# Kernel optimization log

Hardware: AMD Instinct MI355X
Metric: run time of the kernel (lower is better)

## Reference

```python
import jax, jax.numpy as jnp
import numpy as np

NUM_STEPS = 100
STEP = 2.0 / (NUM_STEPS - 1)          # bin width over [-1, 1]
EPS = 1.0 / NUM_STEPS
TSIZE = NUM_STEPS                      # bin centers t_k = -1 + k*STEP, k=0..99
B, D = 4096, 128
NUM_CLASSES = 100


def setup_inputs() -> dict:
    key = jax.random.key(0)
    k1, k2 = jax.random.split(key)
    embeddings = jax.random.normal(k1, (B, D), dtype=jnp.float32)
    classes = jax.random.randint(k2, (B,), 0, NUM_CLASSES)
    return {"embeddings": embeddings, "classes": classes}


def _histogram_loss(embeddings, classes):
    n = embeddings.shape[0]
    iu, ju = np.triu_indices(n, 1)            # static upper-triangular pair indices
    # cosine similarity of all pairs (outer_cosine_similarity)
    en = embeddings / jnp.linalg.norm(embeddings, axis=1, keepdims=True)
    dists = en @ en.T                          # [B, B]
    s = jnp.clip(dists[iu, ju], -1.0 + 1e-6, 1.0 - 1e-6)   # [P]
    pos = (classes[iu] == classes[ju])         # [P] bool

    # soft triangular-kernel 2-bin scatter (equivalent to indsa/indsb masking):
    # bin j gets (t_j + STEP - s)/STEP, bin j+1 gets (s - t_j)/STEP
    j = jnp.floor((s + 1.0 - 1e-6) / STEP).astype(jnp.int32)   # lower bin index
    t_j = j.astype(s.dtype) * STEP - 1.0
    w_hi = (s - t_j) / STEP                    # weight for bin j+1
    w_lo = (t_j + STEP - s) / STEP             # weight for bin j

    def histogram(mask):
        m = mask.astype(s.dtype)
        size = m.sum()
        h = jnp.zeros((TSIZE,), dtype=s.dtype)
        h = h.at[j].add(w_lo * m).at[j + 1].add(w_hi * m)
        return h / size

    hist_pos = histogram(pos)
    hist_neg = histogram(~pos)
    # tril-masked repeat + sum(0) in the original is exactly a cumulative sum
    hist_pos_cdf = jnp.cumsum(hist_pos)
    return jnp.sum(hist_neg * hist_pos_cdf)


def reference(embeddings, classes):
    return _histogram_loss(embeddings, classes)
```

## Files before the change

kernel.cpp:

```cpp
#include <hip/hip_runtime.h>
#include <hip/hip_bf16.h>
#include <cstddef>

#define BN 4096
#define DD 128
#define NSTEPS 100
#define PTILE 128
#define PLSTR 136
#define GRID_T 32
#define NOFF 496
#define NBLK 264
#define NREPH 16
#define NREPC2 8

typedef __attribute__((ext_vector_type(8))) short bf16x8;
typedef __attribute__((ext_vector_type(4))) float f32x4;

__device__ __forceinline__ void faddf(float* p, float v) { unsafeAtomicAdd(p, v); }

#define ZERON 166

__global__ __launch_bounds__(256) void hl_normalize(const float* __restrict__ emb,
                                                    ushort* __restrict__ out,
                                                    float* __restrict__ zero_blk) {
    if (blockIdx.x == 0 && threadIdx.x < ZERON) zero_blk[threadIdx.x] = 0.f;
    int w = threadIdx.x >> 6;
    int lane = threadIdx.x & 63;
    int row = (blockIdx.x << 2) + w;
    const float2 v = *(const float2*)(emb + (size_t)row * DD + 2 * lane);
    float ss = v.x * v.x + v.y * v.y;
    #pragma unroll
    for (int off = 32; off > 0; off >>= 1) ss += __shfl_xor(ss, off);
    float inv = 1.0f / sqrtf(ss);
    __hip_bfloat16 b0 = __float2bfloat16(v.x * inv);
    __hip_bfloat16 b1 = __float2bfloat16(v.y * inv);
    ushort2 pk;
    pk.x = *(ushort*)&b0;
    pk.y = *(ushort*)&b1;
    *(ushort2*)(out + (size_t)row * DD + 2 * lane) = pk;
}

__global__ __launch_bounds__(256) void hl_poscls(const ushort* __restrict__ nemb,
                                                 const int* __restrict__ cls,
                                                 float* __restrict__ gPos,
                                                 unsigned int* __restrict__ gDoneP,
                                                 float* __restrict__ gCdf) {
    const int c = blockIdx.x;
    __shared__ int idx[256];
    __shared__ ushort As[64 * PLSTR];
    __shared__ ushort Bs[64 * PLSTR];
    __shared__ float hpos[NREPH * 101];
    __shared__ int mCnt;
    __shared__ int lastFlag;
    const int tid = threadIdx.x;

    if (tid == 0) mCnt = 0;
    for (int i = tid; i < NREPH * 101; i += 256) hpos[i] = 0.f;
    __syncthreads();

    for (int i = tid; i < BN; i += 256)
        if (cls[i] == c) { int p = atomicAdd(&mCnt, 1); if (p < 256) idx[p] = i; }
    __syncthreads();
    const int m = mCnt > 256 ? 256 : mCnt;
    const int nt = (m + 63) >> 6;

    constexpr float INVSTEP = 49.5f;
    constexpr float CLIPV = 1.0f - 1e-6f;

    const int lane = tid & 63;
    const int wv = tid >> 6;
    const int lr = lane & 15;
    const int kg = lane >> 4;
    const int rep = (lane & 15) * 101;

    for (int si = 0; si < nt; ++si) {
        for (int sj = si; sj < nt; ++sj) {
            __syncthreads();
            #pragma unroll
            for (int it = 0; it < 4; ++it) {
                int q = it * 256 + tid;
                int row = q >> 4;
                int ch = q & 15;
                int ga = si * 64 + row;
                int gb = sj * 64 + row;
                int ra = idx[ga < m ? ga : 0];
                int rb = idx[gb < m ? gb : 0];
                *(float4*)(&As[row * PLSTR + ch * 8]) =
                    *(const float4*)(nemb + (size_t)ra * DD + ch * 8);
                *(float4*)(&Bs[row * PLSTR + ch * 8]) =
                    *(const float4*)(nemb + (size_t)rb * DD + ch * 8);
            }
            __syncthreads();

            f32x4 zero4 = {0.f, 0.f, 0.f, 0.f};
            f32x4 pacc[4] = {zero4, zero4, zero4, zero4};
            #pragma unroll
            for (int ks = 0; ks < 4; ++ks) {
                bf16x8 af = *(const bf16x8*)(&As[(wv * 16 + lr) * PLSTR + ks * 32 + kg * 8]);
                #pragma unroll
                for (int fb = 0; fb < 4; ++fb) {
                    bf16x8 bf = *(const bf16x8*)(&Bs[(fb * 16 + lr) * PLSTR + ks * 32 + kg * 8]);
                    pacc[fb] = __builtin_amdgcn_mfma_f32_16x16x32_bf16(af, bf, pacc[fb], 0, 0, 0);
                }
            }

            #pragma unroll
            for (int fb = 0; fb < 4; ++fb) {
                const int gb = sj * 64 + fb * 16 + lr;
                #pragma unroll
                for (int j = 0; j < 4; ++j) {
                    const int ga = si * 64 + wv * 16 + kg * 4 + j;
                    if (ga < gb && gb < m) {
                        float s = pacc[fb][j];
                        s = fminf(fmaxf(s, -CLIPV), CLIPV);
                        float u = (s + CLIPV) * INVSTEP;
                        int jb = (int)u;
                        if (jb > 98) jb = 98;
                        float w_hi = u - (float)jb;
                        float w_lo = 1.0f - w_hi;
                        faddf(&hpos[rep + jb], w_lo);
                        faddf(&hpos[rep + jb + 1], w_hi);
                    }
                }
            }
        }
    }
    __syncthreads();
    if (tid < NSTEPS) {
        float v = 0.f;
        #pragma unroll
        for (int r = 0; r < NREPH; ++r) v += hpos[r * 101 + tid];
        if (v != 0.f) faddf(&gPos[tid], v);
    }
    __threadfence();
    if (tid == 0) {
        unsigned int tk = atomicAdd(gDoneP, 1u);
        lastFlag = (tk == NSTEPS - 1);
    }
    __syncthreads();
    if (lastFlag) {
        float v = (tid < NSTEPS)
            ? __hip_atomic_load(&gPos[tid], __ATOMIC_RELAXED, __HIP_MEMORY_SCOPE_AGENT) : 0.f;
        if (tid < 128) hpos[tid] = v;
        __syncthreads();
        for (int off = 1; off < 128; off <<= 1) {
            float x = 0.f;
            if (tid < 128 && tid >= off) x = hpos[tid - off];
            __syncthreads();
            if (tid < 128) hpos[tid] += x;
            __syncthreads();
        }
        const float invsp = 1.0f / hpos[NSTEPS - 1];
        if (tid < NSTEPS) gCdf[tid] = hpos[tid] * invsp;
    }
}

__global__ __launch_bounds__(256, 2) void hl_neg(const ushort* __restrict__ nemb,
                                                 const int* __restrict__ cls,
                                                 const float* __restrict__ gCdf,
                                                 float* __restrict__ gLoss,
                                                 float* __restrict__ gCnt,
                                                 unsigned int* __restrict__ gDone,
                                                 float* __restrict__ out) {
    __shared__ ushort As[PTILE * 128];
    __shared__ ushort Bs[PTILE * 128];
    __shared__ float2 cdf2[NREPC2 * 101];
    __shared__ float red[8];
    __shared__ int clsAb[2][PTILE], clsBb[2][PTILE];

    const int tid = threadIdx.x;
    const int lane = tid & 63;
    const int wid = tid >> 6;
    const int wr = wid >> 1, wc = wid & 1;
    const int lr = lane & 15;
    const int kg = lane >> 4;

    int tiU[2], tjU[2];
    #pragma unroll
    for (int u = 0; u < 2; ++u) {
        int id = blockIdx.x * 2 + u;
        if (id < NOFF) {
            int ti = 0, rem = id;
            while (rem >= GRID_T - 1 - ti) { rem -= GRID_T - 1 - ti; ++ti; }
            tiU[u] = ti; tjU[u] = ti + 1 + rem;
        } else {
            tiU[u] = tjU[u] = id - NOFF;
        }
    }

    for (int i = tid; i < NREPC2 * NSTEPS; i += 256) {
        int r = i / NSTEPS, b = i - r * NSTEPS;
        float c0 = gCdf[b];
        float c1 = gCdf[(b < NSTEPS - 1) ? b + 1 : NSTEPS - 1];
        float2 cd; cd.x = c0; cd.y = c1 - c0;
        cdf2[r * 101 + b] = cd;
    }

    constexpr float INVSTEP = 49.5f;
    constexpr float CLIPV = 1.0f - 1e-6f;
    const float2* crep2 = &cdf2[(lane & 7) * 101];
    const int li_base = wr * 64 + (kg << 2);
    const int lj_base = wc * 64 + lr;

    float lacc = 0.f, lcnt = 0.f;
    const int rloc = lane >> 4;
    const int pch = lane & 15;

    #define STAGE_UNIT(U)                                                            \
    {                                                                                \
        const int ti_ = tiU[U], tj_ = tjU[U];                                        \
        const bool dg_ = (ti_ == tj_);                                               \
        if (tid < PTILE) clsAb[(U) & 1][tid] = cls[ti_ * PTILE + tid];               \
        else             clsBb[(U) & 1][tid - PTILE] = cls[tj_ * PTILE + (tid - PTILE)]; \
        const ushort* Ag_ = nemb + (size_t)(ti_ * PTILE) * DD;                       \
        const ushort* Bg_ = nemb + (size_t)(tj_ * PTILE) * DD;                       \
        _Pragma("unroll")                                                            \
        for (int t = 0; t < 8; ++t) {                                                \
            int row = wid * 32 + t * 4 + rloc;                                       \
            int lch = pch ^ (row & 7);                                               \
            const ushort* ga = Ag_ + (size_t)row * DD + lch * 8;                     \
            ushort* la = &As[(wid * 32 + t * 4) * 128];                              \
            __builtin_amdgcn_global_load_lds(                                        \
                (const __attribute__((address_space(1))) void*)ga,                   \
                (__attribute__((address_space(3))) void*)la, 16, 0, 0);              \
        }                                                                            \
        if (!dg_) {                                                                  \
            _Pragma("unroll")                                                        \
            for (int t = 0; t < 8; ++t) {                                            \
                int row = wid * 32 + t * 4 + rloc;                                   \
                int lch = pch ^ (row & 7);                                           \
                const ushort* gb = Bg_ + (size_t)row * DD + lch * 8;                 \
                ushort* lb = &Bs[(wid * 32 + t * 4) * 128];                          \
                __builtin_amdgcn_global_load_lds(                                    \
                    (const __attribute__((address_space(1))) void*)gb,               \
                    (__attribute__((address_space(3))) void*)lb, 16, 0, 0);          \
            }                                                                        \
        }                                                                            \
    }

    STAGE_UNIT(0);

    #pragma unroll
    for (int u = 0; u < 2; ++u) {
        const bool diag = (tiU[u] == tjU[u]);

        __syncthreads();

        const ushort* Bsel = diag ? As : Bs;

        f32x4 zero4 = {0.f, 0.f, 0.f, 0.f};
        f32x4 acc[4][4];
        #pragma unroll
        for (int a = 0; a < 4; ++a)
            #pragma unroll
            for (int b = 0; b < 4; ++b) acc[a][b] = zero4;

        #pragma unroll
        for (int ks = 0; ks < 4; ++ks) {
            bf16x8 af[4], bfr[4];
            #pragma unroll
            for (int f = 0; f < 4; ++f) {
                int arow = wr * 64 + f * 16 + lr;
                int pca = ((ks << 2) | kg) ^ (arow & 7);
                af[f] = *(const bf16x8*)(&As[arow * 128 + pca * 8]);
                int brow = wc * 64 + f * 16 + lr;
                int pcb = ((ks << 2) | kg) ^ (brow & 7);
                bfr[f] = *(const bf16x8*)(&Bsel[brow * 128 + pcb * 8]);
            }
            #pragma unroll
            for (int fa = 0; fa < 4; ++fa)
                #pragma unroll
                for (int fb = 0; fb < 4; ++fb)
                    acc[fa][fb] = __builtin_amdgcn_mfma_f32_16x16x32_bf16(af[fa], bfr[fb], acc[fa][fb], 0, 0, 0);
        }

        __syncthreads();

        if (u == 0) STAGE_UNIT(1);

        const int* clsA_ = clsAb[u & 1];
        const int* clsB_ = diag ? clsAb[u & 1] : clsBb[u & 1];
        const bool offdiag = !diag;

        int ca[16];
        #pragma unroll
        for (int fa = 0; fa < 4; ++fa)
            #pragma unroll
            for (int j = 0; j < 4; ++j) ca[fa * 4 + j] = clsA_[li_base + fa * 16 + j];

        #pragma unroll
        for (int fb = 0; fb < 4; ++fb) {
            const int lj = lj_base + fb * 16;
            const int cb = clsB_[lj];
            #pragma unroll
            for (int fa = 0; fa < 4; ++fa) {
                const int li0 = li_base + fa * 16;
                f32x4 v = acc[fa][fb];
                #pragma unroll
                for (int j = 0; j < 4; ++j) {
                    const int li = li0 + j;
                    const bool mneg = (offdiag || (li < lj)) && (ca[fa * 4 + j] != cb);
                    float s = v[j];
                    s = fminf(fmaxf(s, -CLIPV), CLIPV);
                    float uu = (s + CLIPV) * INVSTEP;
                    int jb = (int)uu;
                    if (jb > 98) jb = 98;
                    float w_hi = uu - (float)jb;
                    float2 cd = crep2[jb];
                    float mm = mneg ? 1.0f : 0.0f;
                    lacc = fmaf(mm, fmaf(w_hi, cd.y, cd.x), lacc);
                    lcnt += mm;
                }
            }
        }
    }
    #undef STAGE_UNIT

    #pragma unroll
    for (int off = 32; off > 0; off >>= 1) {
        lacc += __shfl_xor(lacc, off);
        lcnt += __shfl_xor(lcnt, off);
    }
    if (lane == 0) { red[wid] = lacc; red[4 + wid] = lcnt; }
    __syncthreads();
    if (tid == 0) {
        float L = red[0] + red[1] + red[2] + red[3];
        float C = red[4] + red[5] + red[6] + red[7];
        faddf(&gLoss[blockIdx.x & 31], L);
        faddf(&gCnt[blockIdx.x & 31], C);
        __threadfence();
        unsigned int tk = atomicAdd(gDone, 1u);
        if (tk == NBLK - 1) {
            __threadfence();
            float ls = 0.f, cs = 0.f;
            for (int i = 0; i < 32; ++i) {
                ls += __hip_atomic_load(&gLoss[i], __ATOMIC_RELAXED, __HIP_MEMORY_SCOPE_AGENT);
                cs += __hip_atomic_load(&gCnt[i], __ATOMIC_RELAXED, __HIP_MEMORY_SCOPE_AGENT);
            }
            out[0] = ls / cs;
        }
    }
}

extern "C" void kernel_launch(void* const* d_in, const int* in_sizes, int n_in,
                              void* d_out, int out_size, void* d_ws, size_t ws_size,
                              hipStream_t stream) {
    const float* emb = (const float*)d_in[0];
    const int* classes = (const int*)d_in[1];
    float* out = (float*)d_out;

    ushort* nemb = (ushort*)d_ws;
    float* ctl = (float*)((char*)d_ws + (size_t)BN * DD * sizeof(ushort));
    float* gPos = ctl;
    float* gLoss = gPos + NSTEPS;
    float* gCnt = gLoss + 32;
    unsigned int* gDone = (unsigned int*)(gCnt + 32);
    unsigned int* gDoneP = gDone + 1;
    float* gCdf = (float*)(gDoneP + 1);

    hl_normalize<<<BN / 4, 256, 0, stream>>>(emb, nemb, ctl);
    hl_poscls<<<NSTEPS, 256, 0, stream>>>(nemb, classes, gPos, gDoneP, gCdf);
    hl_neg<<<NBLK, 256, 0, stream>>>(nemb, classes, gCdf, gLoss, gCnt, gDone, out);
}
```

Baseline: 43.46 us.

## Use per-thread fp16 private LDS histograms and reuse A tile on diagonal

Replaces the 16-way replicated float LDS histogram, which was updated with atomics, by a private fp16 histogram per thread (100 bins x 256 threads). Each thread updates its own bins with a branch-free read-modify-write, and the copies are reduced with a skewed access pattern at the end. Diagonal tiles skip loading B and read the A tile instead. The change removes LDS atomic contention and divergence, at the cost of about 51 KB of extra LDS (lower occupancy), fp16 accumulation precision loss, and a larger zeroing and reduction pass. It also adds a dead loop.

```diff
diff --git a/kernel.cpp b/kernel.cpp
--- a/kernel.cpp
+++ b/kernel.cpp
@@ -1,5 +1,6 @@
 #include <hip/hip_runtime.h>
 #include <hip/hip_bf16.h>
+#include <hip/hip_fp16.h>
 #include <cstddef>
 
 #define BN 4096
@@ -10,7 +11,6 @@
 #define GRID_T 32
 #define NOFF 496
 #define NBLK 264
-#define NREPH 16
 #define NREPC2 8
 
 typedef __attribute__((ext_vector_type(8))) short bf16x8;
@@ -49,13 +49,16 @@
     __shared__ int idx[256];
     __shared__ ushort As[64 * PLSTR];
     __shared__ ushort Bs[64 * PLSTR];
-    __shared__ float hpos[NREPH * 101];
+    __shared__ _Float16 hallh[NSTEPS * 256];
+    __shared__ float scanb[128];
     __shared__ int mCnt;
     __shared__ int lastFlag;
+    uint* hall32 = (uint*)hallh;
     const int tid = threadIdx.x;
 
     if (tid == 0) mCnt = 0;
-    for (int i = tid; i < NREPH * 101; i += 256) hpos[i] = 0.f;
+    #pragma unroll 8
+    for (int i = tid; i < NSTEPS * 128; i += 256) hall32[i] = 0u;
     __syncthreads();
 
     for (int i = tid; i < BN; i += 256)
@@ -71,26 +74,42 @@
     const int wv = tid >> 6;
     const int lr = lane & 15;
     const int kg = lane >> 4;
-    const int rep = (lane & 15) * 101;
 
     for (int si = 0; si < nt; ++si) {
         for (int sj = si; sj < nt; ++sj) {
+            const bool same = (sj == si);
             __syncthreads();
+            #pragma unroll
+            for (int it = 0; it < 2; ++it) {
+                int q = it * 256 + tid;
+                int row = q >> 4;
+                (void)row;
+            }
             #pragma unroll
             for (int it = 0; it < 4; ++it) {
                 int q = it * 256 + tid;
                 int row = q >> 4;
                 int ch = q & 15;
                 int ga = si * 64 + row;
-                int gb = sj * 64 + row;
                 int ra = idx[ga < m ? ga : 0];
-                int rb = idx[gb < m ? gb : 0];
                 *(float4*)(&As[row * PLSTR + ch * 8]) =
                     *(const float4*)(nemb + (size_t)ra * DD + ch * 8);
-                *(float4*)(&Bs[row * PLSTR + ch * 8]) =
-                    *(const float4*)(nemb + (size_t)rb * DD + ch * 8);
+            }
+            if (!same) {
+                #pragma unroll
+                for (int it = 0; it < 4; ++it) {
+                    int q = it * 256 + tid;
+                    int row = q >> 4;
+                    int ch = q & 15;
+                    int gb = sj * 64 + row;
+                    int rb = idx[gb < m ? gb : 0];
+                    *(float4*)(&Bs[row * PLSTR + ch * 8]) =
+                        *(const float4*)(nemb + (size_t)rb * DD + ch * 8);
+                }
             }
             __syncthreads();
+
+            const ushort* Bsel = same ? As : Bs;
 
             f32x4 zero4 = {0.f, 0.f, 0.f, 0.f};
             f32x4 pacc[4] = {zero4, zero4, zero4, zero4};
@@ -99,7 +118,7 @@
                 bf16x8 af = *(const bf16x8*)(&As[(wv * 16 + lr) * PLSTR + ks * 32 + kg * 8]);
                 #pragma unroll
                 for (int fb = 0; fb < 4; ++fb) {
-                    bf16x8 bf = *(const bf16x8*)(&Bs[(fb * 16 + lr) * PLSTR + ks * 32 + kg * 8]);
+                    bf16x8 bf = *(const bf16x8*)(&Bsel[(fb * 16 + lr) * PLSTR + ks * 32 + kg * 8]);
                     pacc[fb] = __builtin_amdgcn_mfma_f32_16x16x32_bf16(af, bf, pacc[fb], 0, 0, 0);
                 }
             }
@@ -110,27 +129,46 @@
                 #pragma unroll
                 for (int j = 0; j < 4; ++j) {
                     const int ga = si * 64 + wv * 16 + kg * 4 + j;
-                    if (ga < gb && gb < m) {
-                        float s = pacc[fb][j];
-                        s = fminf(fmaxf(s, -CLIPV), CLIPV);
-                        float u = (s + CLIPV) * INVSTEP;
-                        int jb = (int)u;
-                        if (jb > 98) jb = 98;
-                        float w_hi = u - (float)jb;
-                        float w_lo = 1.0f - w_hi;
-                        faddf(&hpos[rep + jb], w_lo);
-                        faddf(&hpos[rep + jb + 1], w_hi);
-                    }
+                    const bool valid = (ga < gb) && (gb < m);
+                    float s = pacc[fb][j];
+                    s = fminf(fmaxf(s, -CLIPV), CLIPV);
+                    float u = (s + CLIPV) * INVSTEP;
+                    int jb = (int)u;
+                    if (jb > 98) jb = 98;
+                    float vm = valid ? 1.0f : 0.0f;
+                    float w_hi = (u - (float)jb) * vm;
+                    float w_lo = vm - w_hi;
+                    int base = jb * 256 + tid;
+                    _Float16 lo = hallh[base];
+                    _Float16 hi = hallh[base + 256];
+                    hallh[base] = lo + (_Float16)w_lo;
+                    hallh[base + 256] = hi + (_Float16)w_hi;
                 }
             }
         }
     }
     __syncthreads();
+
     if (tid < NSTEPS) {
-        float v = 0.f;
-        #pragma unroll
-        for (int r = 0; r < NREPH; ++r) v += hpos[r * 101 + tid];
-        if (v != 0.f) faddf(&gPos[tid], v);
+        const int b = tid;
+        float ssum = 0.f;
+        #pragma unroll 8
+        for (int r = 0; r < 64; ++r) {
+            uint u2 = hall32[b * 128 + ((r + b) & 127)];
+            __half2 h2 = *(__half2*)&u2;
+            ssum += __low2float(h2) + __high2float(h2);
+        }
+        if (ssum != 0.f) faddf(&gPos[b], ssum);
+    } else if (tid >= 128 && tid < 128 + NSTEPS) {
+        const int b = tid - 128;
+        float ssum = 0.f;
+        #pragma unroll 8
+        for (int r = 64; r < 128; ++r) {
+            uint u2 = hall32[b * 128 + ((r + b) & 127)];
+            __half2 h2 = *(__half2*)&u2;
+            ssum += __low2float(h2) + __high2float(h2);
+        }
+        if (ssum != 0.f) faddf(&gPos[b], ssum);
     }
     __threadfence();
     if (tid == 0) {
@@ -141,17 +179,17 @@
     if (lastFlag) {
         float v = (tid < NSTEPS)
             ? __hip_atomic_load(&gPos[tid], __ATOMIC_RELAXED, __HIP_MEMORY_SCOPE_AGENT) : 0.f;
-        if (tid < 128) hpos[tid] = v;
+        if (tid < 128) scanb[tid] = v;
         __syncthreads();
         for (int off = 1; off < 128; off <<= 1) {
             float x = 0.f;
-            if (tid < 128 && tid >= off) x = hpos[tid - off];
+            if (tid < 128 && tid >= off) x = scanb[tid - off];
             __syncthreads();
-            if (tid < 128) hpos[tid] += x;
+            if (tid < 128) scanb[tid] += x;
             __syncthreads();
         }
-        const float invsp = 1.0f / hpos[NSTEPS - 1];
-        if (tid < NSTEPS) gCdf[tid] = hpos[tid] * invsp;
+        const float invsp = 1.0f / scanb[NSTEPS - 1];
+        if (tid < NSTEPS) gCdf[tid] = scanb[tid] * invsp;
     }
 }
 
```

Measured after the change: 43.75 us. About the same (+0.7%).
